# Kernel tuning notes

Measured on AMD Instinct MI355X. Metric: run time of the kernel, lower is better.

## Reference

```python
import jax, jax.numpy as jnp
import numpy as np

B = 16384
N_HDV = 12
N_CAV = 8
STEP = 344  # one_step_obs_dim
ALPHA = 0.2  # GAT leaky-relu slope
NEG = -9e15

# field offsets inside one 344-dim step: hdv[0:72] cav[72:120] lanes[120:228]
# bottle[228:230] road_end[230:232] target[232:234] self[234:247]
# dist_bott[247:249] dist_end[249:251] exe[251:253] gen[253:254]

def _linear(x, W, b):
    return x @ W + b

def _mlp(x, W1, b1, W2, b2):
    return jax.nn.relu(_linear(jax.nn.relu(_linear(x, W1, b1)), W2, b2))

def _gat_layer(h, adj, W, a):
    # e_ij = leakyrelu(a . [Wh_i ; Wh_j]) computed without NxNx2F materialization
    Wh = h @ W                       # [B,N,F]
    F = W.shape[1]
    s_i = Wh @ a[:F]                 # [B,N]
    s_j = Wh @ a[F:]                 # [B,N]
    e = jax.nn.leaky_relu(s_i[:, :, None] + s_j[:, None, :], ALPHA)
    e = jnp.where(adj > 0, e, NEG)
    att = jax.nn.softmax(e, axis=2)  # dropout is identity in eval mode
    return att @ Wh                  # [B,N,F]

def _gat(x, adj, W1, a1, W2, a2, Wo, ao):
    x = jnp.concatenate([_gat_layer(x, adj, W1, a1), _gat_layer(x, adj, W2, a2)], axis=2)
    x = jax.nn.elu(_gat_layer(x, adj, Wo, ao))
    return x.mean(axis=1)

def _star_adj(n):
    # ones with [1:,1:] zeroed -> ego-star graph (plus self row/col of node 0)
    return jnp.ones((n, n), jnp.float32).at[1:, 1:].set(0.0)

def setup_inputs() -> dict:
    key = jax.random.key(0)
    ks = iter(jax.random.split(key, 40))
    def rn(shape, scale=0.1):
        return jax.random.normal(next(ks), shape, jnp.float32) * scale
    return {
        'obs': rn((B, STEP * 6), 1.0),
        'W_se': rn((15, 64)), 'b_se': jnp.zeros((64,), jnp.float32),
        'W_de': rn((64, 32)), 'b_de': jnp.zeros((32,), jnp.float32),
        'Wh1': rn((32, 64)), 'ah1': rn((128,)),
        'Wh2': rn((32, 64)), 'ah2': rn((128,)),
        'Who': rn((128, 64)), 'aho': rn((128,)),
        'Wc1': rn((6, 16)), 'ac1': rn((32,)),
        'Wc2': rn((6, 16)), 'ac2': rn((32,)),
        'Wco': rn((32, 64)), 'aco': rn((128,)),
        'Wl1': rn((108, 64)), 'bl1': jnp.zeros((64,), jnp.float32),
        'Wl2': rn((64, 64)), 'bl2': jnp.zeros((64,), jnp.float32),
        'Wm1': rn((205, 64)), 'bm1': jnp.zeros((64,), jnp.float32),
        'Wm2': rn((64, 64)), 'bm2': jnp.zeros((64,), jnp.float32),
    }

def reference(obs, W_se, b_se, W_de, b_de, Wh1, ah1, Wh2, ah2, Who, aho,
              Wc1, ac1, Wc2, ac2, Wco, aco, Wl1, bl1, Wl2, bl2, Wm1, bm1, Wm2, bm2):
    chunks = [obs[:, t * STEP:(t + 1) * STEP] for t in range(6)]  # hist5..current
    hist = chunks[1:6]  # hist4, hist3, hist2, hist1, current
    cur = chunks[5]

    ego3 = lambda c: c[:, 234:237]
    hdv3 = lambda c: c[:, 0:72].reshape(-1, N_HDV, 6)[:, :, :3]
    lrelu01 = lambda x: jax.nn.leaky_relu(x, 0.1)

    history_ego = jnp.concatenate([ego3(c)[:, None, :] for c in hist], axis=2)  # [B,1,15]
    history_hdv = jnp.concatenate([hdv3(c) for c in hist], axis=2)              # [B,12,15]

    hist_ego_emb = _linear(lrelu01(_linear(history_ego, W_se, b_se)), W_de, b_de)  # [B,1,32]
    hist_hdv_emb = _linear(lrelu01(_linear(history_hdv, W_se, b_se)), W_de, b_de)  # [B,12,32]

    adj_hdv = _star_adj(N_HDV + 1)
    adj_cav = _star_adj(N_CAV + 1)

    combined_hdv = jnp.concatenate([hist_ego_emb, hist_hdv_emb], axis=1)  # [B,13,32]
    hdv_rel = _gat(combined_hdv, adj_hdv, Wh1, ah1, Wh2, ah2, Who, aho)   # [B,64]

    cav_stats = cur[:, 72:120].reshape(-1, N_CAV, 6)
    ego_action = jnp.concatenate(
        [cur[:, 234:237], cur[:, 253:254], cur[:, 251:253]], axis=1)[:, None, :]  # [B,1,6]
    combined_cav = jnp.concatenate([ego_action, cav_stats], axis=1)        # [B,9,6]
    cav_rel = _gat(combined_cav, adj_cav, Wc1, ac1, Wc2, ac2, Wco, aco)    # [B,64]

    lanes = _mlp(cur[:, 120:228], Wl1, bl1, Wl2, bl2)                      # [B,64]
    road = jnp.concatenate([cur[:, 228:230], cur[:, 247:249], cur[:, 230:232],
                            cur[:, 249:251], cur[:, 232:234]], axis=1)     # [B,10]
    combined = jnp.concatenate(
        [hdv_rel, cav_rel, lanes, road, cur[:, 251:253], cur[:, 253:254]], axis=1)  # [B,205]
    return _mlp(combined, Wm1, bm1, Wm2, bm2)  # [B,64]
```

## Files before the change

kernel.cpp:

```cpp
#include <hip/hip_runtime.h>

#define DEV __device__ __forceinline__

typedef _Float16 h2v __attribute__((ext_vector_type(2)));
typedef _Float16 f16x4v __attribute__((ext_vector_type(4)));
typedef float f32x4v __attribute__((ext_vector_type(4)));

DEV unsigned pk2u(float a, float b) {
    return __builtin_bit_cast(unsigned, __builtin_amdgcn_cvt_pkrtz(a, b));
}
DEV float dot2u(unsigned a, unsigned b, float c) {
#if __has_builtin(__builtin_amdgcn_fdot2)
    return __builtin_amdgcn_fdot2(__builtin_bit_cast(h2v, a),
                                  __builtin_bit_cast(h2v, b), c, false);
#else
    float d;
    asm("v_dot2_f32_f16 %0, %1, %2, %3" : "=v"(d) : "v"(a), "v"(b), "v"(c));
    return d;
#endif
}
DEV f16x4v mk4(unsigned a, unsigned b) {
    union { unsigned u[2]; f16x4v h; } t; t.u[0] = a; t.u[1] = b; return t.h;
}

DEV float wsum64(float v) {
    v += __shfl_xor(v, 32);
    v += __shfl_xor(v, 16);
    v += __shfl_xor(v, 8);
    v += __shfl_xor(v, 4);
    v += __shfl_xor(v, 2);
    v += __shfl_xor(v, 1);
    return v;
}
DEV float lrelu(float x, float a) { return x > 0.f ? x : a * x; }
DEV float elu1(float x) { return x > 0.f ? x : (__expf(x) - 1.f); }

#define OSE 0
#define ODE 512
#define OH1 1536
#define OH2 2560
#define OHO 3584
#define OL1 7680
#define OL2 11136
#define OM1 13184
#define OM2 19840
#define OCO 21888
#define WTOT 22912
#define OHA WTOT
#define OCA (WTOT + 64)
#define WTOT2 (WTOT + 80)
#define F1 WTOT2
#define F2 (F1 + 512)
#define F3 (F2 + 1024)
#define F4 (F3 + 3584)
#define FM1 (F4 + 2048)
#define FM2 (FM1 + 6656)
#define FEND (FM2 + 2048)
#define HSH_WS 40960
#define CV2_WS (HSH_WS + 13 * 16384 * 16)
#define COMB_WS (CV2_WS + 16384 * 32)

__global__ __launch_bounds__(256) void prep_weights(
    const float* __restrict__ W_se, const float* __restrict__ W_de,
    const float* __restrict__ Wh1, const float* __restrict__ Wh2,
    const float* __restrict__ Who, const float* __restrict__ Wl1,
    const float* __restrict__ Wl2, const float* __restrict__ Wm1,
    const float* __restrict__ Wm2, const float* __restrict__ Wco,
    const float* __restrict__ ah1, const float* __restrict__ ah2,
    const float* __restrict__ ac1, const float* __restrict__ ac2,
    const float* __restrict__ Wc1, const float* __restrict__ Wc2,
    const float* __restrict__ b_se, const float* __restrict__ bl1,
    const float* __restrict__ bm1,
    unsigned* __restrict__ ws)
{
    int i = blockIdx.x * 256 + threadIdx.x;
    if (i >= FEND) return;
    if (i >= WTOT2) {
        int i2 = i - WTOT2;
        unsigned val;
        if (i2 < 512) {
            int tile = i2 >> 7, rem = i2 & 127, reg = rem >> 6, lane = rem & 63;
            int m = tile * 16 + (lane & 15);
            int k0 = 4 * (lane >> 4) + reg * 2;
            float v0 = (k0 < 15) ? W_se[k0 * 64 + m] : ((k0 == 15) ? b_se[m] : 0.f);
            float v1 = (k0 + 1 < 15) ? W_se[(k0 + 1) * 64 + m] : ((k0 + 1 == 15) ? b_se[m] : 0.f);
            val = pk2u(v0, v1);
        } else if (i2 < 1536) {
            int j = i2 - 512;
            int tile = j >> 7, rem = j & 127, reg = rem >> 6, lane = rem & 63;
            int mt2 = tile >> 2, kt2 = tile & 3;
            int m = mt2 * 16 + (lane & 15);
            int k0 = kt2 * 16 + 4 * (lane >> 4) + reg * 2;
            val = pk2u(W_de[k0 * 32 + m], W_de[(k0 + 1) * 32 + m]);
        } else if (i2 < 5120) {
            int j = i2 - 1536;
            int tile = j >> 7, rem = j & 127, reg = rem >> 6, lane = rem & 63;
            int mt1 = tile / 7, kt1 = tile % 7;
            int m = mt1 * 16 + (lane & 15);
            int k0 = kt1 * 16 + 4 * (lane >> 4) + reg * 2;
            float v0 = (k0 < 108) ? Wl1[k0 * 64 + m] : ((k0 == 108) ? bl1[m] : 0.f);
            float v1 = (k0 + 1 < 108) ? Wl1[(k0 + 1) * 64 + m] : ((k0 + 1 == 108) ? bl1[m] : 0.f);
            val = pk2u(v0, v1);
        } else if (i2 < 7168) {
            int j = i2 - 5120;
            int tile = j >> 7, rem = j & 127, reg = rem >> 6, lane = rem & 63;
            int mt1 = tile >> 2, kt1 = tile & 3;
            int m = mt1 * 16 + (lane & 15);
            int k0 = kt1 * 16 + 4 * (lane >> 4) + reg * 2;
            val = pk2u(Wl2[k0 * 64 + m], Wl2[(k0 + 1) * 64 + m]);
        } else if (i2 < 13824) {
            int j = i2 - 7168;
            int tile = j >> 7, rem = j & 127, reg = rem >> 6, lane = rem & 63;
            int mt1 = tile / 13, kt1 = tile % 13;
            int m = mt1 * 16 + (lane & 15);
            int k0 = kt1 * 16 + 4 * (lane >> 4) + reg * 2;
            float v0 = (k0 < 205) ? Wm1[k0 * 64 + m] : ((k0 == 205) ? bm1[m] : 0.f);
            float v1 = (k0 + 1 < 205) ? Wm1[(k0 + 1) * 64 + m] : ((k0 + 1 == 205) ? bm1[m] : 0.f);
            val = pk2u(v0, v1);
        } else {
            int j = i2 - 13824;
            int tile = j >> 7, rem = j & 127, reg = rem >> 6, lane = rem & 63;
            int mt1 = tile >> 2, kt1 = tile & 3;
            int m = mt1 * 16 + (lane & 15);
            int k0 = kt1 * 16 + 4 * (lane >> 4) + reg * 2;
            val = pk2u(Wm2[k0 * 64 + m], Wm2[(k0 + 1) * 64 + m]);
        }
        ws[i] = val;
        return;
    }
    if (i >= WTOT) {
        int j = i - WTOT;
        if (j < 64) {
            int vec = j >> 4, c2 = j & 15;
            const float* W = (vec < 2) ? Wh1 : Wh2;
            const float* a = (vec < 2) ? ah1 : ah2;
            int sel = (vec & 1) ? 0 : 64;
            float v0 = 0.f, v1 = 0.f;
            for (int q = 0; q < 64; ++q) {
                v0 += W[(2 * c2) * 64 + q] * a[sel + q];
                v1 += W[(2 * c2 + 1) * 64 + q] * a[sel + q];
            }
            ws[i] = pk2u(v0, v1);
        } else {
            int jj = j - 64;
            int vec = jj >> 2, p = jj & 3;
            const float* W = (vec < 2) ? Wc1 : Wc2;
            const float* a = (vec < 2) ? ac1 : ac2;
            int sel = (vec & 1) ? 0 : 16;
            int k0 = 2 * p, k1 = 2 * p + 1;
            float v0 = 0.f, v1 = 0.f;
            if (k0 < 6) for (int q = 0; q < 16; ++q) v0 += W[k0 * 16 + q] * a[sel + q];
            if (k1 < 6) for (int q = 0; q < 16; ++q) v1 += W[k1 * 16 + q] * a[sel + q];
            ws[i] = pk2u(v0, v1);
        }
        return;
    }
    const float* W; int K, N, j;
    if (i < ODE)      { W = W_se; K = 15;  N = 64; j = i - OSE; }
    else if (i < OH1) { W = W_de; K = 64;  N = 32; j = i - ODE; }
    else if (i < OH2) { W = Wh1;  K = 32;  N = 64; j = i - OH1; }
    else if (i < OHO) { W = Wh2;  K = 32;  N = 64; j = i - OH2; }
    else if (i < OL1) { W = Who;  K = 128; N = 64; j = i - OHO; }
    else if (i < OL2) { W = Wl1;  K = 108; N = 64; j = i - OL1; }
    else if (i < OM1) { W = Wl2;  K = 64;  N = 64; j = i - OL2; }
    else if (i < OM2) { W = Wm1;  K = 205; N = 64; j = i - OM1; }
    else if (i < OCO) { W = Wm2;  K = 64;  N = 64; j = i - OM2; }
    else              { W = Wco;  K = 32;  N = 64; j = i - OCO; }
    int k2 = j / N, n = j % N;
    float v0 = (2 * k2     < K) ? W[(2 * k2)     * N + n] : 0.f;
    float v1 = (2 * k2 + 1 < K) ? W[(2 * k2 + 1) * N + n] : 0.f;
    ws[i] = pk2u(v0, v1);
}

__global__ __launch_bounds__(256) void gemm_pre(
    const float* __restrict__ obs, const unsigned* __restrict__ WS,
    const float* __restrict__ b_de, const float* __restrict__ bl2,
    unsigned* __restrict__ wsh, unsigned* __restrict__ wsc, int split)
{
    const int l = threadIdx.x & 63;
    const int w = threadIdx.x >> 6;
    const int t = blockIdx.x * 4 + w;
    const int lo16 = l & 15, hi4 = l >> 4;

    if (t < split) {
        int g = t * 16 + lo16;
        int e = g / 13, r = g - e * 13;
        const float* o = obs + (size_t)e * 2064;
        unsigned b1[2];
#pragma unroll
        for (int reg = 0; reg < 2; ++reg) {
            float v[2];
#pragma unroll
            for (int h = 0; h < 2; ++h) {
                int k = 4 * hi4 + reg * 2 + h;
                float x;
                if (k < 15) {
                    int tc = k / 3 + 1, ff = k - (k / 3) * 3;
                    int col = (r == 0) ? (234 + ff) : ((r - 1) * 6 + ff);
                    x = o[tc * 344 + col];
                } else x = (k == 15) ? 1.f : 0.f;
                v[h] = x;
            }
            b1[reg] = pk2u(v[0], v[1]);
        }
        f16x4v B1 = mk4(b1[0], b1[1]);
        f32x4v d1[4];
#pragma unroll
        for (int mt = 0; mt < 4; ++mt) {
            f16x4v A = mk4(WS[F1 + mt * 128 + l], WS[F1 + mt * 128 + 64 + l]);
            f32x4v z = {0.f, 0.f, 0.f, 0.f};
            d1[mt] = __builtin_amdgcn_mfma_f32_16x16x16f16(A, B1, z, 0, 0, 0);
        }
        f16x4v B2[4];
#pragma unroll
        for (int kt = 0; kt < 4; ++kt) {
            B2[kt] = mk4(pk2u(lrelu(d1[kt][0], 0.1f), lrelu(d1[kt][1], 0.1f)),
                         pk2u(lrelu(d1[kt][2], 0.1f), lrelu(d1[kt][3], 0.1f)));
        }
#pragma unroll
        for (int mt2 = 0; mt2 < 2; ++mt2) {
            float4 bb = *(const float4*)(b_de + mt2 * 16 + 4 * hi4);
            f32x4v acc = {bb.x, bb.y, bb.z, bb.w};
#pragma unroll
            for (int kt = 0; kt < 4; ++kt) {
                f16x4v A = mk4(WS[F2 + (mt2 * 4 + kt) * 128 + l],
                               WS[F2 + (mt2 * 4 + kt) * 128 + 64 + l]);
                acc = __builtin_amdgcn_mfma_f32_16x16x16f16(A, B2[kt], acc, 0, 0, 0);
            }
            unsigned* dst = wsh + (size_t)g * 16 + mt2 * 8 + 2 * hi4;
            dst[0] = pk2u(acc[0], acc[1]);
            dst[1] = pk2u(acc[2], acc[3]);
        }
    } else {
        int tt = t - split;
        int e = tt * 16 + lo16;
        const float* o = obs + (size_t)e * 2064 + 1840;
        f32x4v acc1[4];
#pragma unroll
        for (int mt = 0; mt < 4; ++mt) acc1[mt] = (f32x4v){0.f, 0.f, 0.f, 0.f};
#pragma unroll
        for (int kt = 0; kt < 7; ++kt) {
            unsigned bu[2];
#pragma unroll
            for (int reg = 0; reg < 2; ++reg) {
                float v[2];
#pragma unroll
                for (int h = 0; h < 2; ++h) {
                    int k = kt * 16 + 4 * hi4 + reg * 2 + h;
                    v[h] = (k < 108) ? o[k] : ((k == 108) ? 1.f : 0.f);
                }
                bu[reg] = pk2u(v[0], v[1]);
            }
            f16x4v Bf = mk4(bu[0], bu[1]);
#pragma unroll
            for (int mt = 0; mt < 4; ++mt) {
                f16x4v A = mk4(WS[F3 + (mt * 7 + kt) * 128 + l],
                               WS[F3 + (mt * 7 + kt) * 128 + 64 + l]);
                acc1[mt] = __builtin_amdgcn_mfma_f32_16x16x16f16(A, Bf, acc1[mt], 0, 0, 0);
            }
        }
        f16x4v B2[4];
#pragma unroll
        for (int kt = 0; kt < 4; ++kt) {
            B2[kt] = mk4(pk2u(fmaxf(acc1[kt][0], 0.f), fmaxf(acc1[kt][1], 0.f)),
                         pk2u(fmaxf(acc1[kt][2], 0.f), fmaxf(acc1[kt][3], 0.f)));
        }
#pragma unroll
        for (int mt = 0; mt < 4; ++mt) {
            float4 bb = *(const float4*)(bl2 + mt * 16 + 4 * hi4);
            f32x4v acc = {bb.x, bb.y, bb.z, bb.w};
#pragma unroll
            for (int kt = 0; kt < 4; ++kt) {
                f16x4v A = mk4(WS[F4 + (mt * 4 + kt) * 128 + l],
                               WS[F4 + (mt * 4 + kt) * 128 + 64 + l]);
                acc = __builtin_amdgcn_mfma_f32_16x16x16f16(A, B2[kt], acc, 0, 0, 0);
            }
            unsigned* dst = wsc + (size_t)e * 32 + mt * 8 + 2 * hi4;
            dst[0] = pk2u(fmaxf(acc[0], 0.f), fmaxf(acc[1], 0.f));
            dst[1] = pk2u(fmaxf(acc[2], 0.f), fmaxf(acc[3], 0.f));
        }
    }
}

__global__ __launch_bounds__(256) void gemm_post(
    const unsigned* __restrict__ WS, const unsigned* __restrict__ combw,
    const float* __restrict__ bm2, float* __restrict__ out)
{
    const int l = threadIdx.x & 63;
    const int w = threadIdx.x >> 6;
    const int t = blockIdx.x * 4 + w;
    const int lo16 = l & 15, hi4 = l >> 4;
    const int e = t * 16 + lo16;
    const unsigned* cw = combw + (size_t)e * 104;

    f32x4v acc1[4];
#pragma unroll
    for (int mt = 0; mt < 4; ++mt) acc1[mt] = (f32x4v){0.f, 0.f, 0.f, 0.f};
#pragma unroll
    for (int kt = 0; kt < 13; ++kt) {
        int j0 = kt * 8 + 2 * hi4;
        f16x4v Bf = mk4(cw[j0], cw[j0 + 1]);
#pragma unroll
        for (int mt = 0; mt < 4; ++mt) {
            f16x4v A = mk4(WS[FM1 + (mt * 13 + kt) * 128 + l],
                           WS[FM1 + (mt * 13 + kt) * 128 + 64 + l]);
            acc1[mt] = __builtin_amdgcn_mfma_f32_16x16x16f16(A, Bf, acc1[mt], 0, 0, 0);
        }
    }
    f16x4v B2[4];
#pragma unroll
    for (int kt = 0; kt < 4; ++kt) {
        B2[kt] = mk4(pk2u(fmaxf(acc1[kt][0], 0.f), fmaxf(acc1[kt][1], 0.f)),
                     pk2u(fmaxf(acc1[kt][2], 0.f), fmaxf(acc1[kt][3], 0.f)));
    }
#pragma unroll
    for (int mt = 0; mt < 4; ++mt) {
        float4 bb = *(const float4*)(bm2 + mt * 16 + 4 * hi4);
        f32x4v acc = {bb.x, bb.y, bb.z, bb.w};
#pragma unroll
        for (int kt = 0; kt < 4; ++kt) {
            f16x4v A = mk4(WS[FM2 + (mt * 4 + kt) * 128 + l],
                           WS[FM2 + (mt * 4 + kt) * 128 + 64 + l]);
            acc = __builtin_amdgcn_mfma_f32_16x16x16f16(A, B2[kt], acc, 0, 0, 0);
        }
        float4 st;
        st.x = fmaxf(acc[0], 0.f);
        st.y = fmaxf(acc[1], 0.f);
        st.z = fmaxf(acc[2], 0.f);
        st.w = fmaxf(acc[3], 0.f);
        *(float4*)(out + (size_t)e * 64 + mt * 16 + 4 * hi4) = st;
    }
}

#define HSHF  0
#define COMBH 128
#define XC0H  296
#define XCRH  312
#define CURS  624
#define HCF   864
#define SCR   936
#define S12H  1000
#define QCF   1032
#define HCH   1048
#define X0S2  1088
#define XRS2  1152
#define HSH2  1216
#define ELEM_U 1480

__global__ __launch_bounds__(256, 4) void pred_kernel(
    const float* __restrict__ obs,
    const unsigned* __restrict__ WS,
    const unsigned* __restrict__ WSH, const unsigned* __restrict__ WSC,
    const float* __restrict__ aho,
    const float* __restrict__ Wc1, const float* __restrict__ Wc2,
    const float* __restrict__ aco,
    unsigned* __restrict__ combw)
{
    const int l = threadIdx.x & 63;
    const int w = threadIdx.x >> 6;
    const int b = blockIdx.x * 4 + w;
    const float* o = obs + (size_t)b * 2064;

    __shared__ unsigned lds[4 * ELEM_U];
    unsigned* SU = lds + w * ELEM_U;
    float* SF = (float*)SU;

    unsigned cv2reg = (l < 32) ? WSC[(size_t)b * 32 + l] : 0u;
    for (int i = l; i < 184; i += 64) SF[CURS + i] = o[1792 + i];
    for (int i = l; i < 208; i += 64) {
        int rr = i >> 4, c2 = i & 15;
        unsigned v = WSH[(size_t)(b * 13 + rr) * 16 + c2];
        SU[HSH2 + rr * 20 + c2] = v;
        union { unsigned u; h2v h; } tc; tc.u = v;
        float2 f2; f2.x = (float)tc.h[0]; f2.y = (float)tc.h[1];
        *(float2*)(SF + HSHF + rr * 32 + 2 * c2) = f2;
    }
    for (int i = l; i < 72; i += 64) {
        int r = i >> 3, f = i & 7;
        float v = 0.f;
        if (f < 6) {
            if (r == 0) {
                int idx = (f < 3) ? (162 + f) : ((f == 3) ? 181 : (175 + f));
                v = SF[CURS + idx];
            } else {
                v = SF[CURS + (r - 1) * 6 + f];
            }
        }
        SF[HCF + i] = v;
    }
    if (l < 36) {
        int r = l >> 2, p = l & 3;
        float v0 = SF[HCF + r * 8 + 2 * p];
        float v1 = SF[HCF + r * 8 + 2 * p + 1];
        SU[HCH + r * 4 + p] = pk2u(v0, v1);
    }

    {
        int g = l >> 4, r = l & 15;
        float sc = 0.f;
        if (g < 2) {
            if (r < 14) {
                int ridx = (r == 13) ? 0 : r;
                const uint4* hr = (const uint4*)(SU + HSH2 + ridx * 20);
                const uint4* av = (const uint4*)(WS + OHA + g * 32 + ((r == 13) ? 16 : 0));
                uint4 h0 = hr[0], h1 = hr[1], h2 = hr[2], h3 = hr[3];
                uint4 a0 = av[0], a1 = av[1], a2 = av[2], a3 = av[3];
                float sa = 0.f, sb = 0.f;
                sa = dot2u(h0.x, a0.x, sa); sa = dot2u(h0.y, a0.y, sa);
                sa = dot2u(h0.z, a0.z, sa); sa = dot2u(h0.w, a0.w, sa);
                sb = dot2u(h1.x, a1.x, sb); sb = dot2u(h1.y, a1.y, sb);
                sb = dot2u(h1.z, a1.z, sb); sb = dot2u(h1.w, a1.w, sb);
                sa = dot2u(h2.x, a2.x, sa); sa = dot2u(h2.y, a2.y, sa);
                sa = dot2u(h2.z, a2.z, sa); sa = dot2u(h2.w, a2.w, sa);
                sb = dot2u(h3.x, a3.x, sb); sb = dot2u(h3.y, a3.y, sb);
                sb = dot2u(h3.z, a3.z, sb); sb = dot2u(h3.w, a3.w, sb);
                sc = sa + sb;
            }
        } else {
            if (r < 10) {
                int ridx = (r == 9) ? 0 : r;
                const uint4* hr = (const uint4*)(SU + HCH + ridx * 4);
                const uint4* cv = (const uint4*)(WS + OCA + (g - 2) * 8 + ((r == 9) ? 4 : 0));
                uint4 h = hr[0];
                uint4 a = cv[0];
                sc = dot2u(h.x, a.x, sc);
                sc = dot2u(h.y, a.y, sc);
                sc = dot2u(h.z, a.z, sc);
            }
        }
        SF[SCR + l] = sc;
    }

    if (l < 32) {
        const float4* sq = (const float4*)(SF + SCR);
        float4 a0 = sq[0], a1 = sq[1], a2 = sq[2], a3 = sq[3];
        float4 b0 = sq[4], b1 = sq[5], b2 = sq[6], b3 = sq[7];
        float p1[13] = {a0.x,a0.y,a0.z,a0.w,a1.x,a1.y,a1.z,a1.w,a2.x,a2.y,a2.z,a2.w,a3.x};
        float si1 = a3.y;
        float p2[13] = {b0.x,b0.y,b0.z,b0.w,b1.x,b1.y,b1.z,b1.w,b2.x,b2.y,b2.z,b2.w,b3.x};
        float si2 = b3.y;
        float m1 = -1e30f, m2 = -1e30f;
#pragma unroll
        for (int r = 0; r < 13; ++r) {
            p1[r] = lrelu(si1 + p1[r], 0.2f);
            p2[r] = lrelu(si2 + p2[r], 0.2f);
            m1 = fmaxf(m1, p1[r]);
            m2 = fmaxf(m2, p2[r]);
        }
        float den1 = 0.f, den2 = 0.f;
#pragma unroll
        for (int r = 0; r < 13; ++r) {
            p1[r] = __expf(p1[r] - m1);
            p2[r] = __expf(p2[r] - m2);
            den1 += p1[r];
            den2 += p2[r];
        }
        float rd1 = 1.f / den1, rd2 = 1.f / den2;
        int c = l;
        float s1 = 0.f, s2 = 0.f;
#pragma unroll
        for (int r = 0; r < 13; ++r) {
            float h = SF[HSHF + r * 32 + c];
            s1 = __builtin_fmaf(p1[r], h, s1);
            s2 = __builtin_fmaf(p2[r], h, s2);
        }
        s1 *= rd1; s2 *= rd2;
        float s1n = __shfl_xor(s1, 1), s2n = __shfl_xor(s2, 1);
        if (!(l & 1)) {
            SU[S12H + (c >> 1)] = pk2u(s1, s1n);
            SU[S12H + 16 + (c >> 1)] = pk2u(s2, s2n);
        }
    } else {
        const float4* sq = (const float4*)(SF + SCR + 32);
        float4 a0 = sq[0], a1 = sq[1], a2 = sq[2];
        float4 b0 = sq[4], b1 = sq[5], b2 = sq[6];
        float q1[9] = {a0.x,a0.y,a0.z,a0.w,a1.x,a1.y,a1.z,a1.w,a2.x};
        float sic1 = a2.y;
        float q2[9] = {b0.x,b0.y,b0.z,b0.w,b1.x,b1.y,b1.z,b1.w,b2.x};
        float sic2 = b2.y;
        float m1 = -1e30f, m2 = -1e30f;
#pragma unroll
        for (int r = 0; r < 9; ++r) {
            q1[r] = lrelu(sic1 + q1[r], 0.2f);
            q2[r] = lrelu(sic2 + q2[r], 0.2f);
            m1 = fmaxf(m1, q1[r]);
            m2 = fmaxf(m2, q2[r]);
        }
        float den1 = 0.f, den2 = 0.f;
#pragma unroll
        for (int r = 0; r < 9; ++r) {
            q1[r] = __expf(q1[r] - m1);
            q2[r] = __expf(q2[r] - m2);
            den1 += q1[r];
            den2 += q2[r];
        }
        float rd1 = 1.f / den1, rd2 = 1.f / den2;
        int k = l & 15;
        int gat = (l >> 4) & 1;
        if (k < 6) {
            float su = 0.f;
#pragma unroll
            for (int r = 0; r < 9; ++r) {
                float h = SF[HCF + r * 8 + k];
                su = __builtin_fmaf(gat ? q2[r] : q1[r], h, su);
            }
            su *= gat ? rd2 : rd1;
            SF[QCF + gat * 8 + k] = su;
        }
    }

    {
        float o1 = 0.f, w1 = 0.f, o2 = 0.f, w2 = 0.f;
        const uint4* s1v = (const uint4*)(SU + S12H);
        const uint4* s2v = (const uint4*)(SU + S12H + 16);
        const uint4* h0v = (const uint4*)(SU + HSH2);
#pragma unroll
        for (int kc = 0; kc < 4; ++kc) {
            uint4 sa = s1v[kc], sb = s2v[kc], hz = h0v[kc];
            unsigned wa0 = WS[OH1 + (kc * 4 + 0) * 64 + l], wb0 = WS[OH2 + (kc * 4 + 0) * 64 + l];
            unsigned wa1 = WS[OH1 + (kc * 4 + 1) * 64 + l], wb1 = WS[OH2 + (kc * 4 + 1) * 64 + l];
            unsigned wa2 = WS[OH1 + (kc * 4 + 2) * 64 + l], wb2 = WS[OH2 + (kc * 4 + 2) * 64 + l];
            unsigned wa3 = WS[OH1 + (kc * 4 + 3) * 64 + l], wb3 = WS[OH2 + (kc * 4 + 3) * 64 + l];
            o1 = dot2u(sa.x, wa0, o1); o1 = dot2u(sa.y, wa1, o1);
            o1 = dot2u(sa.z, wa2, o1); o1 = dot2u(sa.w, wa3, o1);
            w1 = dot2u(hz.x, wa0, w1); w1 = dot2u(hz.y, wa1, w1);
            w1 = dot2u(hz.z, wa2, w1); w1 = dot2u(hz.w, wa3, w1);
            o2 = dot2u(sb.x, wb0, o2); o2 = dot2u(sb.y, wb1, o2);
            o2 = dot2u(sb.z, wb2, o2); o2 = dot2u(sb.w, wb3, o2);
            w2 = dot2u(hz.x, wb0, w2); w2 = dot2u(hz.y, wb1, w2);
            w2 = dot2u(hz.z, wb2, w2); w2 = dot2u(hz.w, wb3, w2);
        }
        float o1n = __shfl_xor(o1, 1), o2n = __shfl_xor(o2, 1);
        float w1n = __shfl_xor(w1, 1), w2n = __shfl_xor(w2, 1);
        if (!(l & 1)) {
            SU[X0S2 + (l >> 1)] = pk2u(o1, o1n);
            SU[X0S2 + 32 + (l >> 1)] = pk2u(o2, o2n);
            SU[XRS2 + (l >> 1)] = pk2u(w1, w1n);
            SU[XRS2 + 32 + (l >> 1)] = pk2u(w2, w2n);
        }
    }

    {
        int g = l >> 4, c = l & 15;
        const float* vec = (g & 1) ? (SF + HCF) : (SF + QCF + (g >> 1) * 8);
        const float* Wc = (g < 2) ? Wc1 : Wc2;
        float acc = 0.f;
#pragma unroll
        for (int k = 0; k < 6; ++k)
            acc = __builtin_fmaf(vec[k], Wc[k * 16 + c], acc);
        float an = __shfl_xor(acc, 1);
        if (!(l & 1))
            SU[((g & 1) ? XCRH : XC0H) + (g >> 1) * 8 + (c >> 1)] = pk2u(acc, an);
    }

    {
        float v = 0.f;
        if (l < 13) {
            int idx;
            if (l < 10) {
                int p = l >> 1, odd = l & 1;
                idx = ((p & 1) ? 175 : 156) + (p >> 1) * 2 + odd;
            } else {
                idx = 169 + l;
            }
            v = SF[CURS + idx];
        } else if (l == 13) {
            v = 1.0f;
        }
        float vn = __shfl_xor(v, 1);
        if (l < 16 && !(l & 1)) SU[COMBH + 96 + (l >> 1)] = pk2u(v, vn);
    }

    float cv0;
    {
        float w0a = 0.f, w0b = 0.f, wra = 0.f, wrb = 0.f;
        const uint4* x4 = (const uint4*)(SU + X0S2);
        const uint4* r4 = (const uint4*)(SU + XRS2);
#pragma unroll 2
        for (int kp = 0; kp < 8; ++kp) {
            int ka = 2 * kp, kb = ka + 1;
            unsigned wk0 = WS[OHO + (ka * 4 + 0) * 64 + l];
            unsigned wk1 = WS[OHO + (ka * 4 + 1) * 64 + l];
            unsigned wk2 = WS[OHO + (ka * 4 + 2) * 64 + l];
            unsigned wk3 = WS[OHO + (ka * 4 + 3) * 64 + l];
            unsigned vk0 = WS[OHO + (kb * 4 + 0) * 64 + l];
            unsigned vk1 = WS[OHO + (kb * 4 + 1) * 64 + l];
            unsigned vk2 = WS[OHO + (kb * 4 + 2) * 64 + l];
            unsigned vk3 = WS[OHO + (kb * 4 + 3) * 64 + l];
            uint4 xa = x4[ka], ra = r4[ka];
            uint4 xb = x4[kb], rb = r4[kb];
            w0a = dot2u(xa.x, wk0, w0a); w0a = dot2u(xa.y, wk1, w0a);
            w0a = dot2u(xa.z, wk2, w0a); w0a = dot2u(xa.w, wk3, w0a);
            wra = dot2u(ra.x, wk0, wra); wra = dot2u(ra.y, wk1, wra);
            wra = dot2u(ra.z, wk2, wra); wra = dot2u(ra.w, wk3, wra);
            w0b = dot2u(xb.x, vk0, w0b); w0b = dot2u(xb.y, vk1, w0b);
            w0b = dot2u(xb.z, vk2, w0b); w0b = dot2u(xb.w, vk3, w0b);
            wrb = dot2u(rb.x, vk0, wrb); wrb = dot2u(rb.y, vk1, wrb);
            wrb = dot2u(rb.z, vk2, wrb); wrb = dot2u(rb.w, vk3, wrb);
        }
        float w0 = w0a + w0b, wr = wra + wrb;
        float si0 = wsum64(w0 * aho[l]);
        float sj0 = wsum64(w0 * aho[64 + l]);
        float sjr = wsum64(wr * aho[64 + l]);
        float e0 = lrelu(si0 + sj0, 0.2f);
        float er = lrelu(si0 + sjr, 0.2f);
        float m = fmaxf(e0, er);
        float p0 = __expf(e0 - m);
        float pr = __expf(er - m) * 12.f;
        float o0 = (p0 * w0 + pr * wr) / (p0 + pr);
        cv0 = (elu1(o0) + 12.f * elu1(w0)) * (1.f / 13.f);
    }
    float cv1;
    {
        float w0 = 0.f, wr = 0.f;
        const uint4* x4 = (const uint4*)(SU + XC0H);
        const uint4* r4 = (const uint4*)(SU + XCRH);
#pragma unroll
        for (int kc = 0; kc < 4; ++kc) {
            uint4 xv = x4[kc], rv = r4[kc];
            unsigned k0 = WS[OCO + (kc * 4 + 0) * 64 + l];
            unsigned k1 = WS[OCO + (kc * 4 + 1) * 64 + l];
            unsigned k2 = WS[OCO + (kc * 4 + 2) * 64 + l];
            unsigned k3 = WS[OCO + (kc * 4 + 3) * 64 + l];
            w0 = dot2u(xv.x, k0, w0); w0 = dot2u(xv.y, k1, w0);
            w0 = dot2u(xv.z, k2, w0); w0 = dot2u(xv.w, k3, w0);
            wr = dot2u(rv.x, k0, wr); wr = dot2u(rv.y, k1, wr);
            wr = dot2u(rv.z, k2, wr); wr = dot2u(rv.w, k3, wr);
        }
        float si0 = wsum64(w0 * aco[l]);
        float sj0 = wsum64(w0 * aco[64 + l]);
        float sjr = wsum64(wr * aco[64 + l]);
        float e0 = lrelu(si0 + sj0, 0.2f);
        float er = lrelu(si0 + sjr, 0.2f);
        float m = fmaxf(e0, er);
        float p0 = __expf(e0 - m);
        float pr = __expf(er - m) * 8.f;
        float o0 = (p0 * w0 + pr * wr) / (p0 + pr);
        cv1 = (elu1(o0) + 8.f * elu1(w0)) * (1.f / 9.f);
    }
    {
        float v0n = __shfl_xor(cv0, 1);
        float v1n = __shfl_xor(cv1, 1);
        if (!(l & 1)) {
            SU[COMBH + (l >> 1)] = pk2u(cv0, v0n);
            SU[COMBH + 32 + (l >> 1)] = pk2u(cv1, v1n);
        }
        if (l < 32) SU[COMBH + 64 + l] = cv2reg;
    }

    {
        unsigned* dst = combw + (size_t)b * 104;
        dst[l] = SU[COMBH + l];
        if (l < 40) dst[64 + l] = SU[COMBH + 64 + l];
    }
}

extern "C" void kernel_launch(void* const* d_in, const int* in_sizes, int n_in,
                              void* d_out, int out_size, void* d_ws, size_t ws_size,
                              hipStream_t stream) {
    const float* obs  = (const float*)d_in[0];
    const float* W_se = (const float*)d_in[1];
    const float* b_se = (const float*)d_in[2];
    const float* W_de = (const float*)d_in[3];
    const float* b_de = (const float*)d_in[4];
    const float* Wh1  = (const float*)d_in[5];
    const float* ah1  = (const float*)d_in[6];
    const float* Wh2  = (const float*)d_in[7];
    const float* ah2  = (const float*)d_in[8];
    const float* Who  = (const float*)d_in[9];
    const float* aho  = (const float*)d_in[10];
    const float* Wc1  = (const float*)d_in[11];
    const float* ac1  = (const float*)d_in[12];
    const float* Wc2  = (const float*)d_in[13];
    const float* ac2  = (const float*)d_in[14];
    const float* Wco  = (const float*)d_in[15];
    const float* aco  = (const float*)d_in[16];
    const float* Wl1  = (const float*)d_in[17];
    const float* bl1  = (const float*)d_in[18];
    const float* Wl2  = (const float*)d_in[19];
    const float* bl2  = (const float*)d_in[20];
    const float* Wm1  = (const float*)d_in[21];
    const float* bm1  = (const float*)d_in[22];
    const float* Wm2  = (const float*)d_in[23];
    const float* bm2  = (const float*)d_in[24];

    unsigned* ws = (unsigned*)d_ws;
    prep_weights<<<(FEND + 255) / 256, 256, 0, stream>>>(
        W_se, W_de, Wh1, Wh2, Who, Wl1, Wl2, Wm1, Wm2, Wco,
        ah1, ah2, ac1, ac2, Wc1, Wc2, b_se, bl1, bm1, ws);

    int B = in_sizes[0] / 2064;
    int t1 = (13 * B) / 16;
    int t2 = B / 16;
    gemm_pre<<<(t1 + t2) / 4, 256, 0, stream>>>(
        obs, ws, b_de, bl2, ws + HSH_WS, ws + CV2_WS, t1);

    pred_kernel<<<B / 4, 256, 0, stream>>>(
        obs, ws, ws + HSH_WS, ws + CV2_WS, aho,
        Wc1, Wc2, aco, ws + COMB_WS);

    gemm_post<<<(B / 16) / 4, 256, 0, stream>>>(
        ws, ws + COMB_WS, bm2, (float*)d_out);
}
```

Measured before the change: 69.33 us.

## Move GAT output-layer projections from per-sample dot2 into batched MFMA final kernel

The per-sample output GAT layers (hdv Who and cav Wco projections, attention scores, softmax, ELU and mean) are moved out of the one-wave-per-sample pred_kernel. They now run in the final GEMM kernel, which processes 16 samples per wave with 16x16x16 f16 MFMA, and the resulting embeddings feed the Wm1 MLP directly from registers. The aim is to replace scalar dot2 loops and 64-lane shuffle reductions with matrix-core work and to drop the combined-vector round trip. In exchange, pred_kernel writes a larger 168-word staging record per sample to global memory, which adds write and read traffic.

Measured after the change: 59.85 us. -13.7%, faster.

```diff
diff --git a/kernel.cpp b/kernel.cpp
--- a/kernel.cpp
+++ b/kernel.cpp
@@ -23,15 +23,6 @@
     union { unsigned u[2]; f16x4v h; } t; t.u[0] = a; t.u[1] = b; return t.h;
 }
 
-DEV float wsum64(float v) {
-    v += __shfl_xor(v, 32);
-    v += __shfl_xor(v, 16);
-    v += __shfl_xor(v, 8);
-    v += __shfl_xor(v, 4);
-    v += __shfl_xor(v, 2);
-    v += __shfl_xor(v, 1);
-    return v;
-}
 DEV float lrelu(float x, float a) { return x > 0.f ? x : a * x; }
 DEV float elu1(float x) { return x > 0.f ? x : (__expf(x) - 1.f); }
 
@@ -55,10 +46,13 @@
 #define F4 (F3 + 3584)
 #define FM1 (F4 + 2048)
 #define FM2 (FM1 + 6656)
-#define FEND (FM2 + 2048)
-#define HSH_WS 40960
+#define FHO (FM2 + 2048)
+#define FCO2 (FHO + 4096)
+#define FEND2 (FCO2 + 1024)
+#define HSH_WS 49152
 #define CV2_WS (HSH_WS + 13 * 16384 * 16)
-#define COMB_WS (CV2_WS + 16384 * 32)
+#define STG_WS (CV2_WS + 16384 * 32)
+#define STG_N 168
 
 __global__ __launch_bounds__(256) void prep_weights(
     const float* __restrict__ W_se, const float* __restrict__ W_de,
@@ -74,7 +68,7 @@
     unsigned* __restrict__ ws)
 {
     int i = blockIdx.x * 256 + threadIdx.x;
-    if (i >= FEND) return;
+    if (i >= FEND2) return;
     if (i >= WTOT2) {
         int i2 = i - WTOT2;
         unsigned val;
@@ -117,13 +111,27 @@
             float v0 = (k0 < 205) ? Wm1[k0 * 64 + m] : ((k0 == 205) ? bm1[m] : 0.f);
             float v1 = (k0 + 1 < 205) ? Wm1[(k0 + 1) * 64 + m] : ((k0 + 1 == 205) ? bm1[m] : 0.f);
             val = pk2u(v0, v1);
-        } else {
+        } else if (i2 < 15872) {
             int j = i2 - 13824;
             int tile = j >> 7, rem = j & 127, reg = rem >> 6, lane = rem & 63;
             int mt1 = tile >> 2, kt1 = tile & 3;
             int m = mt1 * 16 + (lane & 15);
             int k0 = kt1 * 16 + 4 * (lane >> 4) + reg * 2;
             val = pk2u(Wm2[k0 * 64 + m], Wm2[(k0 + 1) * 64 + m]);
+        } else if (i2 < 19968) {
+            int j = i2 - 15872;
+            int tile = j >> 7, rem = j & 127, reg = rem >> 6, lane = rem & 63;
+            int mt1 = tile >> 3, kt1 = tile & 7;
+            int m = mt1 * 16 + (lane & 15);
+            int k0 = kt1 * 16 + 4 * (lane >> 4) + reg * 2;
+            val = pk2u(Who[k0 * 64 + m], Who[(k0 + 1) * 64 + m]);
+        } else {
+            int j = i2 - 19968;
+            int tile = j >> 7, rem = j & 127, reg = rem >> 6, lane = rem & 63;
+            int mt1 = tile >> 1, kt1 = tile & 1;
+            int m = mt1 * 16 + (lane & 15);
+            int k0 = kt1 * 16 + 4 * (lane >> 4) + reg * 2;
+            val = pk2u(Wco[k0 * 64 + m], Wco[(k0 + 1) * 64 + m]);
         }
         ws[i] = val;
         return;
@@ -282,8 +290,10 @@
     }
 }
 
-__global__ __launch_bounds__(256) void gemm_post(
-    const unsigned* __restrict__ WS, const unsigned* __restrict__ combw,
+__global__ __launch_bounds__(256) void gemm_final(
+    const unsigned* __restrict__ WS, const unsigned* __restrict__ stg,
+    const unsigned* __restrict__ wsc,
+    const float* __restrict__ aho, const float* __restrict__ aco,
     const float* __restrict__ bm2, float* __restrict__ out)
 {
     const int l = threadIdx.x & 63;
@@ -291,20 +301,124 @@
     const int t = blockIdx.x * 4 + w;
     const int lo16 = l & 15, hi4 = l >> 4;
     const int e = t * 16 + lo16;
-    const unsigned* cw = combw + (size_t)e * 104;
+    const unsigned* sv = stg + (size_t)e * STG_N;
+
+    f16x4v Bm[13];
+
+    {
+        f32x4v a0[4], a1[4];
+#pragma unroll
+        for (int mt = 0; mt < 4; ++mt) {
+            a0[mt] = (f32x4v){0.f, 0.f, 0.f, 0.f};
+            a1[mt] = (f32x4v){0.f, 0.f, 0.f, 0.f};
+        }
+#pragma unroll
+        for (int kt = 0; kt < 8; ++kt) {
+            f16x4v B0 = mk4(sv[kt * 8 + 2 * hi4], sv[kt * 8 + 2 * hi4 + 1]);
+            f16x4v Br = mk4(sv[64 + kt * 8 + 2 * hi4], sv[64 + kt * 8 + 2 * hi4 + 1]);
+#pragma unroll
+            for (int mt = 0; mt < 4; ++mt) {
+                f16x4v A = mk4(WS[FHO + (mt * 8 + kt) * 128 + l],
+                               WS[FHO + (mt * 8 + kt) * 128 + 64 + l]);
+                a0[mt] = __builtin_amdgcn_mfma_f32_16x16x16f16(A, B0, a0[mt], 0, 0, 0);
+                a1[mt] = __builtin_amdgcn_mfma_f32_16x16x16f16(A, Br, a1[mt], 0, 0, 0);
+            }
+        }
+        float si = 0.f, sj = 0.f, sr = 0.f;
+#pragma unroll
+        for (int mt = 0; mt < 4; ++mt) {
+            float4 AL = *(const float4*)(aho + mt * 16 + 4 * hi4);
+            float4 AH = *(const float4*)(aho + 64 + mt * 16 + 4 * hi4);
+            si += a0[mt][0] * AL.x + a0[mt][1] * AL.y + a0[mt][2] * AL.z + a0[mt][3] * AL.w;
+            sj += a0[mt][0] * AH.x + a0[mt][1] * AH.y + a0[mt][2] * AH.z + a0[mt][3] * AH.w;
+            sr += a1[mt][0] * AH.x + a1[mt][1] * AH.y + a1[mt][2] * AH.z + a1[mt][3] * AH.w;
+        }
+        si += __shfl_xor(si, 16); si += __shfl_xor(si, 32);
+        sj += __shfl_xor(sj, 16); sj += __shfl_xor(sj, 32);
+        sr += __shfl_xor(sr, 16); sr += __shfl_xor(sr, 32);
+        float e0 = lrelu(si + sj, 0.2f);
+        float er = lrelu(si + sr, 0.2f);
+        float m = fmaxf(e0, er);
+        float p0 = __expf(e0 - m);
+        float pr = __expf(er - m) * 12.f;
+        float inv = 1.f / (p0 + pr);
+#pragma unroll
+        for (int mt = 0; mt < 4; ++mt) {
+            float cv[4];
+#pragma unroll
+            for (int r = 0; r < 4; ++r) {
+                float o0 = (p0 * a0[mt][r] + pr * a1[mt][r]) * inv;
+                cv[r] = (elu1(o0) + 12.f * elu1(a0[mt][r])) * (1.f / 13.f);
+            }
+            Bm[mt] = mk4(pk2u(cv[0], cv[1]), pk2u(cv[2], cv[3]));
+        }
+    }
+
+    {
+        f32x4v c0[4], c1[4];
+#pragma unroll
+        for (int mt = 0; mt < 4; ++mt) {
+            c0[mt] = (f32x4v){0.f, 0.f, 0.f, 0.f};
+            c1[mt] = (f32x4v){0.f, 0.f, 0.f, 0.f};
+        }
+#pragma unroll
+        for (int kt = 0; kt < 2; ++kt) {
+            f16x4v B0 = mk4(sv[128 + kt * 8 + 2 * hi4], sv[128 + kt * 8 + 2 * hi4 + 1]);
+            f16x4v Br = mk4(sv[144 + kt * 8 + 2 * hi4], sv[144 + kt * 8 + 2 * hi4 + 1]);
+#pragma unroll
+            for (int mt = 0; mt < 4; ++mt) {
+                f16x4v A = mk4(WS[FCO2 + (mt * 2 + kt) * 128 + l],
+                               WS[FCO2 + (mt * 2 + kt) * 128 + 64 + l]);
+                c0[mt] = __builtin_amdgcn_mfma_f32_16x16x16f16(A, B0, c0[mt], 0, 0, 0);
+                c1[mt] = __builtin_amdgcn_mfma_f32_16x16x16f16(A, Br, c1[mt], 0, 0, 0);
+            }
+        }
+        float si = 0.f, sj = 0.f, sr = 0.f;
+#pragma unroll
+        for (int mt = 0; mt < 4; ++mt) {
+            float4 AL = *(const float4*)(aco + mt * 16 + 4 * hi4);
+            float4 AH = *(const float4*)(aco + 64 + mt * 16 + 4 * hi4);
+            si += c0[mt][0] * AL.x + c0[mt][1] * AL.y + c0[mt][2] * AL.z + c0[mt][3] * AL.w;
+            sj += c0[mt][0] * AH.x + c0[mt][1] * AH.y + c0[mt][2] * AH.z + c0[mt][3] * AH.w;
+            sr += c1[mt][0] * AH.x + c1[mt][1] * AH.y + c1[mt][2] * AH.z + c1[mt][3] * AH.w;
+        }
+        si += __shfl_xor(si, 16); si += __shfl_xor(si, 32);
+        sj += __shfl_xor(sj, 16); sj += __shfl_xor(sj, 32);
+        sr += __shfl_xor(sr, 16); sr += __shfl_xor(sr, 32);
+        float e0 = lrelu(si + sj, 0.2f);
+        float er = lrelu(si + sr, 0.2f);
+        float m = fmaxf(e0, er);
+        float p0 = __expf(e0 - m);
+        float pr = __expf(er - m) * 8.f;
+        float inv = 1.f / (p0 + pr);
+#pragma unroll
+        for (int mt = 0; mt < 4; ++mt) {
+            float cv[4];
+#pragma unroll
+            for (int r = 0; r < 4; ++r) {
+                float o0 = (p0 * c0[mt][r] + pr * c1[mt][r]) * inv;
+                cv[r] = (elu1(o0) + 8.f * elu1(c0[mt][r])) * (1.f / 9.f);
+            }
+            Bm[4 + mt] = mk4(pk2u(cv[0], cv[1]), pk2u(cv[2], cv[3]));
+        }
+    }
+
+#pragma unroll
+    for (int kt = 8; kt < 12; ++kt)
+        Bm[kt] = mk4(wsc[(size_t)e * 32 + (kt - 8) * 8 + 2 * hi4],
+                     wsc[(size_t)e * 32 + (kt - 8) * 8 + 2 * hi4 + 1]);
+    Bm[12] = mk4(sv[160 + 2 * hi4], sv[160 + 2 * hi4 + 1]);
 
     f32x4v acc1[4];
 #pragma unroll
     for (int mt = 0; mt < 4; ++mt) acc1[mt] = (f32x4v){0.f, 0.f, 0.f, 0.f};
 #pragma unroll
     for (int kt = 0; kt < 13; ++kt) {
-        int j0 = kt * 8 + 2 * hi4;
-        f16x4v Bf = mk4(cw[j0], cw[j0 + 1]);
 #pragma unroll
         for (int mt = 0; mt < 4; ++mt) {
             f16x4v A = mk4(WS[FM1 + (mt * 13 + kt) * 128 + l],
                            WS[FM1 + (mt * 13 + kt) * 128 + 64 + l]);
-            acc1[mt] = __builtin_amdgcn_mfma_f32_16x16x16f16(A, Bf, acc1[mt], 0, 0, 0);
+            acc1[mt] = __builtin_amdgcn_mfma_f32_16x16x16f16(A, Bm[kt], acc1[mt], 0, 0, 0);
         }
     }
     f16x4v B2[4];
@@ -333,39 +447,32 @@
 }
 
 #define HSHF  0
-#define COMBH 128
-#define XC0H  296
-#define XCRH  312
 #define CURS  624
 #define HCF   864
 #define SCR   936
 #define S12H  1000
 #define QCF   1032
 #define HCH   1048
-#define X0S2  1088
-#define XRS2  1152
 #define HSH2  1216
 #define ELEM_U 1480
 
 __global__ __launch_bounds__(256, 4) void pred_kernel(
     const float* __restrict__ obs,
     const unsigned* __restrict__ WS,
-    const unsigned* __restrict__ WSH, const unsigned* __restrict__ WSC,
-    const float* __restrict__ aho,
+    const unsigned* __restrict__ WSH,
     const float* __restrict__ Wc1, const float* __restrict__ Wc2,
-    const float* __restrict__ aco,
-    unsigned* __restrict__ combw)
+    unsigned* __restrict__ STG)
 {
     const int l = threadIdx.x & 63;
     const int w = threadIdx.x >> 6;
     const int b = blockIdx.x * 4 + w;
     const float* o = obs + (size_t)b * 2064;
+    unsigned* stg = STG + (size_t)b * STG_N;
 
     __shared__ unsigned lds[4 * ELEM_U];
     unsigned* SU = lds + w * ELEM_U;
     float* SF = (float*)SU;
 
-    unsigned cv2reg = (l < 32) ? WSC[(size_t)b * 32 + l] : 0u;
     for (int i = l; i < 184; i += 64) SF[CURS + i] = o[1792 + i];
     for (int i = l; i < 208; i += 64) {
         int rr = i >> 4, c2 = i & 15;
@@ -533,10 +640,10 @@
         float o1n = __shfl_xor(o1, 1), o2n = __shfl_xor(o2, 1);
         float w1n = __shfl_xor(w1, 1), w2n = __shfl_xor(w2, 1);
         if (!(l & 1)) {
-            SU[X0S2 + (l >> 1)] = pk2u(o1, o1n);
-            SU[X0S2 + 32 + (l >> 1)] = pk2u(o2, o2n);
-            SU[XRS2 + (l >> 1)] = pk2u(w1, w1n);
-            SU[XRS2 + 32 + (l >> 1)] = pk2u(w2, w2n);
+            stg[(l >> 1)] = pk2u(o1, o1n);
+            stg[32 + (l >> 1)] = pk2u(o2, o2n);
+            stg[64 + (l >> 1)] = pk2u(w1, w1n);
+            stg[96 + (l >> 1)] = pk2u(w2, w2n);
         }
     }
 
@@ -550,7 +657,7 @@
             acc = __builtin_fmaf(vec[k], Wc[k * 16 + c], acc);
         float an = __shfl_xor(acc, 1);
         if (!(l & 1))
-            SU[((g & 1) ? XCRH : XC0H) + (g >> 1) * 8 + (c >> 1)] = pk2u(acc, an);
+            stg[128 + ((g & 1) ? 16 : 0) + (g >> 1) * 8 + (c >> 1)] = pk2u(acc, an);
     }
 
     {
@@ -568,90 +675,7 @@
             v = 1.0f;
         }
         float vn = __shfl_xor(v, 1);
-        if (l < 16 && !(l & 1)) SU[COMBH + 96 + (l >> 1)] = pk2u(v, vn);
-    }
-
-    float cv0;
-    {
-        float w0a = 0.f, w0b = 0.f, wra = 0.f, wrb = 0.f;
-        const uint4* x4 = (const uint4*)(SU + X0S2);
-        const uint4* r4 = (const uint4*)(SU + XRS2);
-#pragma unroll 2
-        for (int kp = 0; kp < 8; ++kp) {
-            int ka = 2 * kp, kb = ka + 1;
-            unsigned wk0 = WS[OHO + (ka * 4 + 0) * 64 + l];
-            unsigned wk1 = WS[OHO + (ka * 4 + 1) * 64 + l];
-            unsigned wk2 = WS[OHO + (ka * 4 + 2) * 64 + l];
-            unsigned wk3 = WS[OHO + (ka * 4 + 3) * 64 + l];
-            unsigned vk0 = WS[OHO + (kb * 4 + 0) * 64 + l];
-            unsigned vk1 = WS[OHO + (kb * 4 + 1) * 64 + l];
-            unsigned vk2 = WS[OHO + (kb * 4 + 2) * 64 + l];
-            unsigned vk3 = WS[OHO + (kb * 4 + 3) * 64 + l];
-            uint4 xa = x4[ka], ra = r4[ka];
-            uint4 xb = x4[kb], rb = r4[kb];
-            w0a = dot2u(xa.x, wk0, w0a); w0a = dot2u(xa.y, wk1, w0a);
-            w0a = dot2u(xa.z, wk2, w0a); w0a = dot2u(xa.w, wk3, w0a);
-            wra = dot2u(ra.x, wk0, wra); wra = dot2u(ra.y, wk1, wra);
-            wra = dot2u(ra.z, wk2, wra); wra = dot2u(ra.w, wk3, wra);
-            w0b = dot2u(xb.x, vk0, w0b); w0b = dot2u(xb.y, vk1, w0b);
-            w0b = dot2u(xb.z, vk2, w0b); w0b = dot2u(xb.w, vk3, w0b);
-            wrb = dot2u(rb.x, vk0, wrb); wrb = dot2u(rb.y, vk1, wrb);
-            wrb = dot2u(rb.z, vk2, wrb); wrb = dot2u(rb.w, vk3, wrb);
-        }
-        float w0 = w0a + w0b, wr = wra + wrb;
-        float si0 = wsum64(w0 * aho[l]);
-        float sj0 = wsum64(w0 * aho[64 + l]);
-        float sjr = wsum64(wr * aho[64 + l]);
-        float e0 = lrelu(si0 + sj0, 0.2f);
-        float er = lrelu(si0 + sjr, 0.2f);
-        float m = fmaxf(e0, er);
-        float p0 = __expf(e0 - m);
-        float pr = __expf(er - m) * 12.f;
-        float o0 = (p0 * w0 + pr * wr) / (p0 + pr);
-        cv0 = (elu1(o0) + 12.f * elu1(w0)) * (1.f / 13.f);
-    }
-    float cv1;
-    {
-        float w0 = 0.f, wr = 0.f;
-        const uint4* x4 = (const uint4*)(SU + XC0H);
-        const uint4* r4 = (const uint4*)(SU + XCRH);
-#pragma unroll
-        for (int kc = 0; kc < 4; ++kc) {
-            uint4 xv = x4[kc], rv = r4[kc];
-            unsigned k0 = WS[OCO + (kc * 4 + 0) * 64 + l];
-            unsigned k1 = WS[OCO + (kc * 4 + 1) * 64 + l];
-            unsigned k2 = WS[OCO + (kc * 4 + 2) * 64 + l];
-            unsigned k3 = WS[OCO + (kc * 4 + 3) * 64 + l];
-            w0 = dot2u(xv.x, k0, w0); w0 = dot2u(xv.y, k1, w0);
-            w0 = dot2u(xv.z, k2, w0); w0 = dot2u(xv.w, k3, w0);
-            wr = dot2u(rv.x, k0, wr); wr = dot2u(rv.y, k1, wr);
-            wr = dot2u(rv.z, k2, wr); wr = dot2u(rv.w, k3, wr);
-        }
-        float si0 = wsum64(w0 * aco[l]);
-        float sj0 = wsum64(w0 * aco[64 + l]);
-        float sjr = wsum64(wr * aco[64 + l]);
-        float e0 = lrelu(si0 + sj0, 0.2f);
-        float er = lrelu(si0 + sjr, 0.2f);
-        float m = fmaxf(e0, er);
-        float p0 = __expf(e0 - m);
-        float pr = __expf(er - m) * 8.f;
-        float o0 = (p0 * w0 + pr * wr) / (p0 + pr);
-        cv1 = (elu1(o0) + 8.f * elu1(w0)) * (1.f / 9.f);
-    }
-    {
-        float v0n = __shfl_xor(cv0, 1);
-        float v1n = __shfl_xor(cv1, 1);
-        if (!(l & 1)) {
-            SU[COMBH + (l >> 1)] = pk2u(cv0, v0n);
-            SU[COMBH + 32 + (l >> 1)] = pk2u(cv1, v1n);
-        }
-        if (l < 32) SU[COMBH + 64 + l] = cv2reg;
-    }
-
-    {
-        unsigned* dst = combw + (size_t)b * 104;
-        dst[l] = SU[COMBH + l];
-        if (l < 40) dst[64 + l] = SU[COMBH + 64 + l];
+        if (l < 16 && !(l & 1)) stg[160 + (l >> 1)] = pk2u(v, vn);
     }
 }
 
@@ -685,7 +709,7 @@
     const float* bm2  = (const float*)d_in[24];
 
     unsigned* ws = (unsigned*)d_ws;
-    prep_weights<<<(FEND + 255) / 256, 256, 0, stream>>>(
+    prep_weights<<<(FEND2 + 255) / 256, 256, 0, stream>>>(
         W_se, W_de, Wh1, Wh2, Who, Wl1, Wl2, Wm1, Wm2, Wco,
         ah1, ah2, ac1, ac2, Wc1, Wc2, b_se, bl1, bm1, ws);
 
@@ -696,9 +720,8 @@
         obs, ws, b_de, bl2, ws + HSH_WS, ws + CV2_WS, t1);
 
     pred_kernel<<<B / 4, 256, 0, stream>>>(
-        obs, ws, ws + HSH_WS, ws + CV2_WS, aho,
-        Wc1, Wc2, aco, ws + COMB_WS);
-
-    gemm_post<<<(B / 16) / 4, 256, 0, stream>>>(
-        ws, ws + COMB_WS, bm2, (float*)d_out);
+        obs, ws, ws + HSH_WS, Wc1, Wc2, ws + STG_WS);
+
+    gemm_final<<<(B / 16) / 4, 256, 0, stream>>>(
+        ws, ws + STG_WS, ws + CV2_WS, aho, aco, bm2, (float*)d_out);
 }
```
